# Kernel tuning notes

Hardware: AMD Instinct MI355X
Metric: run time of the kernel (lower is better)

## Reference

```python
import jax, jax.numpy as jnp
import numpy as np

FEATURE_SIZE = 1_000_000
FIELD_SIZE = 39
DIM = 16
BATCH = 8192
CROSS = FIELD_SIZE * (FIELD_SIZE - 1) // 2  # 741


def _pair_index():
    # [[i, j] for i in range(F-1) for j in range(i+1, F)] -> [CROSS, 2]
    idx = [[i, j] for i in range(FIELD_SIZE - 1) for j in range(i + 1, FIELD_SIZE)]
    return jnp.asarray(np.array(idx, dtype=np.int32))


def setup_inputs() -> dict:
    key = jax.random.key(0)
    k1, k2, k3, k4 = jax.random.split(key, 4)
    inputs = jax.random.randint(k1, (BATCH, FIELD_SIZE), 0, FEATURE_SIZE, dtype=jnp.int32)
    embedding_weights = jax.random.normal(k2, (FEATURE_SIZE, DIM), dtype=jnp.float32) * 0.05
    field_weights = jax.random.normal(k3, (CROSS, 1), dtype=jnp.float32) * 0.1
    linear_weights = jax.random.normal(k4, (FEATURE_SIZE,), dtype=jnp.float32) * 0.05
    bias_weight = jnp.zeros((), dtype=jnp.float32)
    return {
        "inputs": inputs,
        "embedding_weights": embedding_weights,
        "field_weights": field_weights,
        "linear_weights": linear_weights,
        "bias_weight": bias_weight,
    }


def reference(inputs, embedding_weights, field_weights, linear_weights, bias_weight):
    pair_idx = _pair_index()  # [CROSS, 2]

    # first order: sum of linear weights over fields -> [B, 1]
    first_order = jnp.sum(linear_weights[inputs], axis=1, keepdims=True)
    bias = jnp.ones_like(first_order) * bias_weight

    # gather each field's embedding once, then index the pairs (same math as
    # the double gather in the original, avoids re-gathering the big table)
    field_emb = embedding_weights[inputs]            # [B, F, D]
    e_i = field_emb[:, pair_idx[:, 0], :]            # [B, CROSS, D]
    e_j = field_emb[:, pair_idx[:, 1], :]            # [B, CROSS, D]
    second_items = jnp.sum(e_i * e_j, axis=-1)       # [B, CROSS]
    second_order = second_items @ field_weights      # [B, 1]

    return bias + first_order + second_order
```

## Files before the change

kernel.cpp:

```cpp
#include <hip/hip_runtime.h>
#include <utility>

#define FIELD 39
#define DIM   16
#define BATCH 8192
#define EPAD  42

constexpr int widx(int i, int j) { return i*(FIELD-1) - i*(i-1)/2 + (j-i-1); }
constexpr int ceil4(int x) { return (x+3) & ~3; }
constexpr int rowlen(int i) { return ceil4(FIELD - 1 - i); }
constexpr int rowstart(int i) {
    int s = 0; for (int m = 0; m < i; ++m) s += rowlen(m); return s;
}
constexpr int WTOT = rowstart(FIELD - 1);

struct WMap { int v[WTOT]; };
constexpr WMap make_map() {
    WMap m{};
    for (int i = 0; i < WTOT; ++i) m.v[i] = -1;
    for (int i = 0; i < FIELD - 1; ++i)
        for (int k = 0; k < FIELD - 1 - i; ++k)
            m.v[rowstart(i) + k] = widx(i, i + 1 + k);
    return m;
}
__device__ constexpr WMap g_map = make_map();

__device__ __forceinline__ float4 ld4(const float* lds, int ofs) {
    return *reinterpret_cast<const float4*>(lds + ofs);
}
template <int EB>
__device__ __forceinline__ float fma4(float4 w, const float (&e)[EPAD], float s) {
    s = fmaf(w.x, e[EB+0], s); s = fmaf(w.y, e[EB+1], s);
    s = fmaf(w.z, e[EB+2], s); s = fmaf(w.w, e[EB+3], s);
    return s;
}
template <int I, size_t... Qs>
__device__ __forceinline__ float row_sum(const float* lds, const float (&e)[EPAD],
                                         std::index_sequence<Qs...>) {
    float s = 0.f;
    ((s = fma4<I + 1 + 4*(int)Qs>(ld4(lds, rowstart(I) + 4*(int)Qs), e, s)), ...);
    return s;
}
template <size_t... Is>
__device__ __forceinline__ float pair_sum(const float* lds, const float (&e)[EPAD],
                                          std::index_sequence<Is...>) {
    float acc[4] = {0.f, 0.f, 0.f, 0.f};
    ((acc[Is & 3] = fmaf(e[Is],
         row_sum<(int)Is>(lds, e, std::make_index_sequence<(size_t)(rowlen((int)Is)/4)>{}),
         acc[Is & 3])), ...);
    return (acc[0] + acc[1]) + (acc[2] + acc[3]);
}
template <size_t... Fs>
__device__ __forceinline__ void gather_all(const int (&idx)[FIELD],
                                           const float* __restrict__ emb,
                                           int d, float (&e)[EPAD],
                                           std::index_sequence<Fs...>) {
    ((e[Fs] = __builtin_nontemporal_load(emb + (size_t)idx[Fs] * DIM + d)), ...);
}
template <size_t... Fs>
__device__ __forceinline__ void load_idx(const int* __restrict__ rowIdx,
                                         int (&idx)[FIELD], std::index_sequence<Fs...>) {
    ((idx[Fs] = rowIdx[Fs]), ...);
}

__global__ __launch_bounds__(256, 2) void fwfm_kernel(
    const int*   __restrict__ inputs,
    const float* __restrict__ emb,
    const float* __restrict__ fw,
    const float* __restrict__ lw,
    const float* __restrict__ bias,
    float*       __restrict__ out)
{
    __shared__ __align__(16) float wlds[WTOT];

    const int tid  = threadIdx.x;
    const int lane = tid & 63;
    const int wave = tid >> 6;
    const int d    = lane & 15;
    const int rloc = lane >> 4;
    const int row  = blockIdx.x * 16 + wave * 4 + rloc;

    const int* rowIdx = inputs + row * FIELD;

    int idx[FIELD];
    load_idx(rowIdx, idx, std::make_index_sequence<FIELD>{});
    float e[EPAD];
    gather_all(idx, emb, d, e, std::make_index_sequence<FIELD>{});
    e[39] = 0.f; e[40] = 0.f; e[41] = 0.f;

    float l0 = lw[idx[d]], l1 = lw[idx[d + 16]];
    float l2 = (d < 7) ? lw[idx[d + 32]] : 0.f;

    for (int s = tid; s < WTOT; s += 256) {
        int m = g_map.v[s];
        wlds[s] = (m >= 0) ? fw[m] : 0.f;
    }
    __syncthreads();

    float so = pair_sum(wlds, e, std::make_index_sequence<FIELD - 1>{});

    float tot = so + (l0 + l1 + l2);
    tot += __shfl_xor(tot, 1, 64);
    tot += __shfl_xor(tot, 2, 64);
    tot += __shfl_xor(tot, 4, 64);
    tot += __shfl_xor(tot, 8, 64);

    if (d == 0) out[row] = tot + bias[0];
}

extern "C" void kernel_launch(void* const* d_in, const int* in_sizes, int n_in,
                              void* d_out, int out_size, void* d_ws, size_t ws_size,
                              hipStream_t stream) {
    const int*   inputs = (const int*)  d_in[0];
    const float* emb    = (const float*)d_in[1];
    const float* fw     = (const float*)d_in[2];
    const float* lw     = (const float*)d_in[3];
    const float* bias   = (const float*)d_in[4];
    float*       out    = (float*)      d_out;

    dim3 grid(BATCH / 16);
    fwfm_kernel<<<grid, 256, 0, stream>>>(inputs, emb, fw, lw, bias, out);
}
```

Baseline: 118.8 us.

## Process two embedding dims per thread with 8-byte gathers, 8 rows per wave

Each thread now owns two embedding dimensions, loaded as one 8-byte gather instead of two 4-byte loads. A wave therefore covers 8 rows instead of 4, and the grid is halved. Each LDS weight float4 is reused for two FMAs, which cuts LDS traffic per pair and the number of cross-lane reduction steps. In exchange, registers per thread roughly double (launch bounds lowered to 1 block per CU), which may reduce occupancy and latency hiding for the random gathers; the nontemporal hint on the embedding loads is also dropped.

After: 113.1 us. -4.8%, faster.

```diff
diff --git a/kernel.cpp b/kernel.cpp
--- a/kernel.cpp
+++ b/kernel.cpp
@@ -5,6 +5,7 @@
 #define DIM   16
 #define BATCH 8192
 #define EPAD  42
+#define RPW   8
 
 constexpr int widx(int i, int j) { return i*(FIELD-1) - i*(i-1)/2 + (j-i-1); }
 constexpr int ceil4(int x) { return (x+3) & ~3; }
@@ -25,45 +26,52 @@
 }
 __device__ constexpr WMap g_map = make_map();
 
+struct f2 { float x, y; };
+
 __device__ __forceinline__ float4 ld4(const float* lds, int ofs) {
     return *reinterpret_cast<const float4*>(lds + ofs);
 }
 template <int EB>
-__device__ __forceinline__ float fma4(float4 w, const float (&e)[EPAD], float s) {
-    s = fmaf(w.x, e[EB+0], s); s = fmaf(w.y, e[EB+1], s);
-    s = fmaf(w.z, e[EB+2], s); s = fmaf(w.w, e[EB+3], s);
-    return s;
+__device__ __forceinline__ void fma4(float4 w, const f2 (&e)[EPAD], f2& s) {
+    s.x = fmaf(w.x, e[EB+0].x, s.x); s.y = fmaf(w.x, e[EB+0].y, s.y);
+    s.x = fmaf(w.y, e[EB+1].x, s.x); s.y = fmaf(w.y, e[EB+1].y, s.y);
+    s.x = fmaf(w.z, e[EB+2].x, s.x); s.y = fmaf(w.z, e[EB+2].y, s.y);
+    s.x = fmaf(w.w, e[EB+3].x, s.x); s.y = fmaf(w.w, e[EB+3].y, s.y);
 }
 template <int I, size_t... Qs>
-__device__ __forceinline__ float row_sum(const float* lds, const float (&e)[EPAD],
-                                         std::index_sequence<Qs...>) {
-    float s = 0.f;
-    ((s = fma4<I + 1 + 4*(int)Qs>(ld4(lds, rowstart(I) + 4*(int)Qs), e, s)), ...);
+__device__ __forceinline__ f2 row_sum(const float* lds, const f2 (&e)[EPAD],
+                                      std::index_sequence<Qs...>) {
+    f2 s{0.f, 0.f};
+    ((fma4<I + 1 + 4*(int)Qs>(ld4(lds, rowstart(I) + 4*(int)Qs), e, s)), ...);
     return s;
 }
 template <size_t... Is>
-__device__ __forceinline__ float pair_sum(const float* lds, const float (&e)[EPAD],
-                                          std::index_sequence<Is...>) {
-    float acc[4] = {0.f, 0.f, 0.f, 0.f};
-    ((acc[Is & 3] = fmaf(e[Is],
-         row_sum<(int)Is>(lds, e, std::make_index_sequence<(size_t)(rowlen((int)Is)/4)>{}),
-         acc[Is & 3])), ...);
-    return (acc[0] + acc[1]) + (acc[2] + acc[3]);
-}
-template <size_t... Fs>
-__device__ __forceinline__ void gather_all(const int (&idx)[FIELD],
-                                           const float* __restrict__ emb,
-                                           int d, float (&e)[EPAD],
-                                           std::index_sequence<Fs...>) {
-    ((e[Fs] = __builtin_nontemporal_load(emb + (size_t)idx[Fs] * DIM + d)), ...);
+__device__ __forceinline__ f2 pair_sum(const float* lds, const f2 (&e)[EPAD],
+                                       std::index_sequence<Is...>) {
+    f2 acc0{0.f, 0.f}, acc1{0.f, 0.f};
+    ((void)[&]{
+        f2 inner = row_sum<(int)Is>(lds, e,
+                       std::make_index_sequence<(size_t)(rowlen((int)Is)/4)>{});
+        f2& a = (Is & 1) ? acc1 : acc0;
+        a.x = fmaf(e[Is].x, inner.x, a.x);
+        a.y = fmaf(e[Is].y, inner.y, a.y);
+    }(), ...);
+    return f2{acc0.x + acc1.x, acc0.y + acc1.y};
 }
 template <size_t... Fs>
 __device__ __forceinline__ void load_idx(const int* __restrict__ rowIdx,
                                          int (&idx)[FIELD], std::index_sequence<Fs...>) {
     ((idx[Fs] = rowIdx[Fs]), ...);
 }
+template <size_t... Fs>
+__device__ __forceinline__ void gather_all(const int (&idx)[FIELD],
+                                           const float* __restrict__ emb,
+                                           int dh2, f2 (&e)[EPAD],
+                                           std::index_sequence<Fs...>) {
+    ((e[Fs] = *reinterpret_cast<const f2*>(emb + (size_t)idx[Fs] * DIM + dh2)), ...);
+}
 
-__global__ __launch_bounds__(256, 2) void fwfm_kernel(
+__global__ __launch_bounds__(256, 1) void fwfm_kernel(
     const int*   __restrict__ inputs,
     const float* __restrict__ emb,
     const float* __restrict__ fw,
@@ -76,20 +84,20 @@
     const int tid  = threadIdx.x;
     const int lane = tid & 63;
     const int wave = tid >> 6;
-    const int d    = lane & 15;
-    const int rloc = lane >> 4;
-    const int row  = blockIdx.x * 16 + wave * 4 + rloc;
+    const int dh   = lane & 7;
+    const int rloc = lane >> 3;
+    const int row  = blockIdx.x * 32 + wave * RPW + rloc;
 
     const int* rowIdx = inputs + row * FIELD;
 
     int idx[FIELD];
     load_idx(rowIdx, idx, std::make_index_sequence<FIELD>{});
-    float e[EPAD];
-    gather_all(idx, emb, d, e, std::make_index_sequence<FIELD>{});
-    e[39] = 0.f; e[40] = 0.f; e[41] = 0.f;
+    f2 e[EPAD];
+    gather_all(idx, emb, dh * 2, e, std::make_index_sequence<FIELD>{});
+    e[39] = f2{0.f, 0.f}; e[40] = f2{0.f, 0.f}; e[41] = f2{0.f, 0.f};
 
-    float l0 = lw[idx[d]], l1 = lw[idx[d + 16]];
-    float l2 = (d < 7) ? lw[idx[d + 32]] : 0.f;
+    float fo = lw[idx[dh]] + lw[idx[dh + 8]] + lw[idx[dh + 16]] + lw[idx[dh + 24]];
+    if (dh < 7) fo += lw[idx[dh + 32]];
 
     for (int s = tid; s < WTOT; s += 256) {
         int m = g_map.v[s];
@@ -97,15 +105,14 @@
     }
     __syncthreads();
 
-    float so = pair_sum(wlds, e, std::make_index_sequence<FIELD - 1>{});
+    f2 so = pair_sum(wlds, e, std::make_index_sequence<FIELD - 1>{});
 
-    float tot = so + (l0 + l1 + l2);
+    float tot = so.x + so.y + fo;
     tot += __shfl_xor(tot, 1, 64);
     tot += __shfl_xor(tot, 2, 64);
     tot += __shfl_xor(tot, 4, 64);
-    tot += __shfl_xor(tot, 8, 64);
 
-    if (d == 0) out[row] = tot + bias[0];
+    if (dh == 0) out[row] = tot + bias[0];
 }
 
 extern "C" void kernel_launch(void* const* d_in, const int* in_sizes, int n_in,
@@ -118,6 +125,6 @@
     const float* bias   = (const float*)d_in[4];
     float*       out    = (float*)      d_out;
 
-    dim3 grid(BATCH / 16);
+    dim3 grid(BATCH / 32);
     fwfm_kernel<<<grid, 256, 0, stream>>>(inputs, emb, fw, lw, bias, out);
 }
```
